# Kernel optimization log

Hardware: AMD Instinct MI355X
Metric: run time of the kernel (lower is better)

The kernel has to match this reference:

```python
import jax, jax.numpy as jnp
import numpy as np

B = 2            # batch size
GRID = 256       # BEV grid H = W
M = 30000        # number of pillars (voxels)
NPTS = 200000    # number of points
IN_C = 16
VOXEL = 0.4      # voxel_size[:2]
PC_MIN = -51.2   # pc_range[:2]
DS = 2           # prod(ds_layer_strides)


def _bn(x, g, b):
    # eval-mode BatchNorm with running_mean=0, running_var=1 (eps absorbed into g)
    return x * g + b


def _conv(x, k, stride):
    # 3x3 conv, padding=1 (spconv SparseConv2d / SubMConv2d with pad k//2), NHWC
    return jax.lax.conv_general_dilated(
        x, k, (stride, stride), ((1, 1), (1, 1)),
        dimension_numbers=('NHWC', 'HWIO', 'NHWC'))


def _active_mask(occ, stride):
    # active output sites of a sparse conv = any active input in the 3x3 receptive field
    pooled = jax.lax.reduce_window(occ, -jnp.inf, jax.lax.max,
                                   (1, 3, 3, 1), (1, stride, stride, 1),
                                   ((0, 0), (1, 1), (1, 1), (0, 0)))
    return (pooled > 0).astype(occ.dtype)


def _forward(features, pfn_w0, pfn_g0, pfn_b0, pfn_w1, pfn_g1, pfn_b1,
             b1_kd, b1_gd, b1_bd, b1_k1, b1_g1, b1_b1, b1_k2, b1_g2, b1_b2,
             b2_kd, b2_gd, b2_bd, b2_k1, b2_g1, b2_b1, b2_k2, b2_g2, b2_b2,
             unq, unq_inv, grid_size):
    # pillar mode: cols 0:2 are xy; convert to (fractional) voxel coordinates
    pos = (features[:, :2] - PC_MIN) / VOXEL  # [N,2] = (px, py)

    # PFN layer 0 (not last): linear(16->16) + BN + ReLU, concat per-pillar max
    h = jax.nn.relu(_bn(features @ pfn_w0, pfn_g0, pfn_b0))            # [N,16]
    hmax = jax.ops.segment_max(h, unq_inv, num_segments=M)             # [M,16]
    h = jnp.concatenate([h, hmax[unq_inv]], axis=1)                    # [N,32]
    # PFN layer 1 (last): linear(32->64) + BN + ReLU
    h = jax.nn.relu(_bn(h @ pfn_w1, pfn_g1, pfn_b1))                   # [N,64]

    # scatter_max pooling points -> pillars
    fv = jax.ops.segment_max(h, unq_inv, num_segments=M)               # [M,64]

    Hn = grid_size
    img = jnp.zeros((B, Hn, Hn, fv.shape[1]), fv.dtype)
    img = img.at[unq[:, 0], unq[:, 1], unq[:, 2]].set(fv)              # dense BEV, NHWC
    occ = jnp.zeros((B, Hn, Hn, 1), fv.dtype)
    occ = occ.at[unq[:, 0], unq[:, 1], unq[:, 2]].set(1.0)

    # block 1: SparseConvBlock(stride=1) + SparseBasicBlock (dense math, masked to active sites)
    occ1 = _active_mask(occ, 1)
    x = jax.nn.relu(_bn(_conv(img, b1_kd, 1), b1_gd, b1_bd)) * occ1
    y = jax.nn.relu(_bn(_conv(x, b1_k1, 1), b1_g1, b1_b1)) * occ1
    y = _bn(_conv(y, b1_k2, 1), b1_g2, b1_b2) * occ1
    x = jax.nn.relu(x + y)

    # block 2: SparseConvBlock(stride=2) + SparseBasicBlock
    occ2 = _active_mask(occ1, 2)
    x = jax.nn.relu(_bn(_conv(x, b2_kd, 2), b2_gd, b2_bd)) * occ2
    y = jax.nn.relu(_bn(_conv(x, b2_k1, 1), b2_g1, b2_b1)) * occ2
    y = _bn(_conv(y, b2_k2, 1), b2_g2, b2_b2) * occ2
    x = jax.nn.relu(x + y)                                             # [B,H/2,W/2,128]

    # bilinear gather at per-point downsampled positions (px -> W axis, py -> H axis)
    bidx = unq[unq_inv, 0]
    px = pos[:, 0] / DS
    py = pos[:, 1] / DS
    Hc, Wc = x.shape[1], x.shape[2]
    x0 = jnp.clip(jnp.floor(px).astype(jnp.int32), 0, Wc - 1)
    x1 = jnp.clip(jnp.floor(px).astype(jnp.int32) + 1, 0, Wc - 1)
    y0 = jnp.clip(jnp.floor(py).astype(jnp.int32), 0, Hc - 1)
    y1 = jnp.clip(jnp.floor(py).astype(jnp.int32) + 1, 0, Hc - 1)
    Ia = x[bidx, y0, x0]
    Ib = x[bidx, y1, x0]
    Ic = x[bidx, y0, x1]
    Id = x[bidx, y1, x1]
    x0f, x1f = x0.astype(px.dtype), x1.astype(px.dtype)
    y0f, y1f = y0.astype(py.dtype), y1.astype(py.dtype)
    wa = ((x1f - px) * (y1f - py))[:, None]
    wb = ((x1f - px) * (py - y0f))[:, None]
    wc = ((px - x0f) * (y1f - py))[:, None]
    wd = ((px - x0f) * (py - y0f))[:, None]
    return Ia * wa + Ib * wb + Ic * wc + Id * wd                       # [N,128]


def setup_inputs() -> dict:
    rng = np.random.default_rng(0)
    d = {}
    d['features'] = jnp.asarray(rng.standard_normal((NPTS, IN_C)).astype(np.float32))
    # unique voxel coords (batch, y, x)
    lin = rng.choice(B * GRID * GRID, size=M, replace=False)
    d['unq'] = jnp.asarray(np.stack([lin // (GRID * GRID), (lin // GRID) % GRID, lin % GRID], 1).astype(np.int32))
    # every pillar gets at least one point
    d['unq_inv'] = jnp.asarray(np.concatenate([np.arange(M), rng.integers(0, M, NPTS - M)]).astype(np.int32))
    d['grid_size'] = GRID

    def w(*s):
        fan = int(np.prod(s[:-1]))
        return jnp.asarray((rng.standard_normal(s) / np.sqrt(fan)).astype(np.float32))

    def g(c):
        return jnp.asarray((0.5 + 0.5 * rng.random(c)).astype(np.float32))

    def bb(c):
        return jnp.asarray((0.1 * rng.standard_normal(c)).astype(np.float32))

    d['pfn_w0'] = w(IN_C, 16); d['pfn_g0'] = g(16); d['pfn_b0'] = bb(16)
    d['pfn_w1'] = w(32, 64);   d['pfn_g1'] = g(64); d['pfn_b1'] = bb(64)
    d['b1_kd'] = w(3, 3, 64, 64);   d['b1_gd'] = g(64);  d['b1_bd'] = bb(64)
    d['b1_k1'] = w(3, 3, 64, 64);   d['b1_g1'] = g(64);  d['b1_b1'] = bb(64)
    d['b1_k2'] = w(3, 3, 64, 64);   d['b1_g2'] = g(64);  d['b1_b2'] = bb(64)
    d['b2_kd'] = w(3, 3, 64, 128);  d['b2_gd'] = g(128); d['b2_bd'] = bb(128)
    d['b2_k1'] = w(3, 3, 128, 128); d['b2_g1'] = g(128); d['b2_b1'] = bb(128)
    d['b2_k2'] = w(3, 3, 128, 128); d['b2_g2'] = g(128); d['b2_b2'] = bb(128)
    return d


def reference(features, unq, unq_inv, grid_size,
              pfn_w0, pfn_g0, pfn_b0, pfn_w1, pfn_g1, pfn_b1,
              b1_kd, b1_gd, b1_bd, b1_k1, b1_g1, b1_b1, b1_k2, b1_g2, b1_b2,
              b2_kd, b2_gd, b2_bd, b2_k1, b2_g1, b2_b1, b2_k2, b2_g2, b2_b2):
    return _forward(features, pfn_w0, pfn_g0, pfn_b0, pfn_w1, pfn_g1, pfn_b1,
                    b1_kd, b1_gd, b1_bd, b1_k1, b1_g1, b1_b1, b1_k2, b1_g2, b1_b2,
                    b2_kd, b2_gd, b2_bd, b2_k1, b2_g1, b2_b1, b2_k2, b2_g2, b2_b2,
                    unq, unq_inv, grid_size)
```

## Files before the change

### kernel.cpp

```cpp
#include <hip/hip_runtime.h>
#include <hip/hip_bf16.h>

#define NPTS    200000
#define MPIL    30000
#define BATCH   2
#define GRID0   256
#define PCMIN   (-51.2f)
#define VOXEL0  (0.4f)
#define NCHUNK  118

#define SLOT_B  ((size_t)16777216)
#define SLOT_F  ((size_t)33554432)

#define W0F 0
#define W1F 256
#define FB1 9216
#define FB2 156672
#define FB3 304128
#define FB4 451584
#define FB5 746496
#define FB6 1336320

#define WS_FLAG 0
#define WS_OCC8 64
#define WS_OCC1 (64 + 131072)
#define WS_OCC2 (64 + 262144)
#define WS_HMAX 393280
#define WS_CNT  2313280
#define WS_OFF  2433280
#define WS_CUR  2553344
#define WS_IDX  2673344
#define WS_LOC  3473344
#define WS_BS   3593344
#define WS_FX   393344

typedef __attribute__((ext_vector_type(8))) short v8s;
typedef __attribute__((ext_vector_type(4))) float f32x4;

static __device__ __forceinline__ float b2f(__hip_bfloat16 v) { return __bfloat162float(v); }
static __device__ __forceinline__ unsigned short f2bbits(float f) {
    __hip_bfloat16 h = __float2bfloat16(f);
    union { __hip_bfloat16 h; unsigned short u; } cv; cv.h = h; return cv.u;
}
static __device__ __forceinline__ float bits2f(unsigned short h) {
    union { unsigned int u; float f; } c; c.u = ((unsigned int)h) << 16; return c.f;
}
static __device__ __forceinline__ float lo2f(unsigned int u) {
    union { unsigned int u; float f; } c; c.u = u << 16; return c.f;
}
static __device__ __forceinline__ float hi2f(unsigned int u) {
    union { unsigned int u; float f; } c; c.u = u & 0xFFFF0000u; return c.f;
}
static __device__ __forceinline__ unsigned int pack2(float a, float b) {
    return (unsigned int)f2bbits(a) | ((unsigned int)f2bbits(b) << 16);
}
static __device__ __forceinline__ void split2(float a, float b, unsigned int& hi, unsigned int& lo) {
    unsigned short ha = f2bbits(a), hb = f2bbits(b);
    hi = (unsigned int)ha | ((unsigned int)hb << 16);
    float ra = a - bits2f(ha);
    float rb = b - bits2f(hb);
    lo = (unsigned int)f2bbits(ra) | ((unsigned int)f2bbits(rb) << 16);
}

static __device__ __forceinline__ float ldf(const void* p, size_t i, int isb) {
    return isb ? b2f(((const __hip_bfloat16*)p)[i]) : ((const float*)p)[i];
}
static __device__ __forceinline__ float4 ld4(const void* p, size_t i, int isb) {
    if (isb) {
        uint2 r = *(const uint2*)((const __hip_bfloat16*)p + i);
        return make_float4(lo2f(r.x), hi2f(r.x), lo2f(r.y), hi2f(r.y));
    }
    return *(const float4*)((const float*)p + i);
}
static __device__ __forceinline__ void st4(void* p, size_t i, int isb, float4 v) {
    if (isb) {
        uint2 pk; pk.x = pack2(v.x, v.y); pk.y = pack2(v.z, v.w);
        *(uint2*)((__hip_bfloat16*)p + i) = pk;
    } else {
        *(float4*)((float*)p + i) = v;
    }
}
static __device__ __forceinline__ void* actptr(void* ob, int slot, int isb) {
    return (char*)ob + (size_t)slot * (isb ? SLOT_B : SLOT_F);
}
static __device__ __forceinline__ float* wpool(void* ob, int isb) {
    return (float*)((char*)ob + 3 * (isb ? SLOT_B : SLOT_F));
}

__global__ void probe_kernel(const unsigned short* __restrict__ g0, int* __restrict__ flag) {
    if (threadIdx.x == 0 && blockIdx.x == 0) {
        int ok = 1;
        for (int i = 0; i < 8; i++) {
            unsigned short u = g0[i];
            if (u < 0x3E00 || u >= 0x4000) ok = 0;
        }
        *flag = ok;
    }
}

__global__ __launch_bounds__(256) void cvt_kernel(const void* __restrict__ src, void* ob,
                                                  int woff, int n, const int* __restrict__ flag) {
    int isb = *flag;
    int i = blockIdx.x * 256 + threadIdx.x;
    if (i < n) wpool(ob, isb)[woff + i] = ldf(src, i, isb);
}

__global__ __launch_bounds__(256) void wfrag_kernel(const void* __restrict__ src, void* ob,
                                                    int fb_bytes, int CIN, int COUT,
                                                    const int* __restrict__ flag)
{
    const int isb = *flag;
    const int cnt = 9 * CIN * COUT;
    int e = blockIdx.x * 256 + threadIdx.x;
    if (e >= cnt) return;
    int i = e & 7;
    int l = (e >> 3) & 63;
    int f = e >> 9;
    int nbn = COUT >> 4, kcn = CIN >> 5;
    int nb = f % nbn;
    int kc = (f / nbn) % kcn;
    int tap = f / (nbn * kcn);
    int ci = kc * 32 + (l >> 4) * 8 + i;
    int co = nb * 16 + (l & 15);
    float wv = ldf(src, (size_t)(tap * CIN + ci) * COUT + co, isb);
    unsigned short h = f2bbits(wv);
    float rem = wv - bits2f(h);
    short* wh = (short*)((char*)ob + 3 * (isb ? SLOT_B : SLOT_F) + fb_bytes);
    wh[e] = (short)h;
    wh[cnt + e] = (short)f2bbits(rem);
}

__global__ __launch_bounds__(256) void hist_kernel(const int* __restrict__ unq_inv,
                                                   int* __restrict__ cnt)
{
    int n = blockIdx.x * 256 + threadIdx.x;
    if (n < NPTS) atomicAdd(&cnt[unq_inv[n]], 1);
}

__global__ __launch_bounds__(256) void scan1_kernel(const int* __restrict__ cnt,
                                                    int* __restrict__ loc,
                                                    int* __restrict__ bs)
{
    __shared__ int s[256];
    const int tid = threadIdx.x;
    const int i = blockIdx.x * 256 + tid;
    int v = (i < MPIL) ? cnt[i] : 0;
    s[tid] = v;
    __syncthreads();
#pragma unroll
    for (int d = 1; d < 256; d <<= 1) {
        int t = (tid >= d) ? s[tid - d] : 0;
        __syncthreads();
        s[tid] += t;
        __syncthreads();
    }
    if (i < MPIL) loc[i] = s[tid] - v;
    if (tid == 255) bs[blockIdx.x] = s[255];
}

__global__ __launch_bounds__(128) void scan2_kernel(int* __restrict__ bs)
{
    __shared__ int s[NCHUNK];
    const int tid = threadIdx.x;
    for (int i = tid; i < NCHUNK; i += 128) s[i] = bs[i];
    __syncthreads();
    if (tid == 0) {
        int acc = 0;
        for (int i = 0; i < NCHUNK; i++) { int t = s[i]; s[i] = acc; acc += t; }
    }
    __syncthreads();
    for (int i = tid; i < NCHUNK; i += 128) bs[i] = s[i];
}

__global__ __launch_bounds__(256) void scan3_kernel(const int* __restrict__ loc,
                                                    const int* __restrict__ bs,
                                                    int* __restrict__ off,
                                                    int* __restrict__ cur)
{
    int i = blockIdx.x * 256 + threadIdx.x;
    if (i < MPIL) {
        int e = loc[i] + bs[blockIdx.x];
        off[i] = e; cur[i] = e;
    }
    if (i == 0) off[MPIL] = NPTS;
}

__global__ __launch_bounds__(256) void fill_kernel(const int* __restrict__ unq_inv,
                                                   int* __restrict__ cur,
                                                   int* __restrict__ idxarr)
{
    int n = blockIdx.x * 256 + threadIdx.x;
    if (n >= NPTS) return;
    int p = unq_inv[n];
    int s = atomicAdd(&cur[p], 1);
    idxarr[s] = n;
}

__global__ __launch_bounds__(256) void pfn0_kernel(
    const void* __restrict__ feat, void* ob, const void* __restrict__ g0,
    const void* __restrict__ b0, const int* __restrict__ flag)
{
    const int isb = *flag;
    int n = blockIdx.x * 256 + threadIdx.x;
    if (n >= NPTS) return;
    const float* w0f = wpool(ob, isb) + W0F;
    void* h0 = actptr(ob, 1, isb);
    float f[16];
#pragma unroll
    for (int i = 0; i < 16; i += 4) {
        float4 v = ld4(feat, (size_t)n * 16 + i, isb);
        f[i] = v.x; f[i + 1] = v.y; f[i + 2] = v.z; f[i + 3] = v.w;
    }
#pragma unroll
    for (int co = 0; co < 16; co += 4) {
        float a0 = 0.f, a1 = 0.f, a2 = 0.f, a3 = 0.f;
#pragma unroll
        for (int ci = 0; ci < 16; ci++) {
            float4 w = *(const float4*)&w0f[ci * 16 + co];
            a0 += f[ci] * w.x; a1 += f[ci] * w.y; a2 += f[ci] * w.z; a3 += f[ci] * w.w;
        }
        float o[4] = { a0, a1, a2, a3 };
#pragma unroll
        for (int k = 0; k < 4; k++) {
            float z = o[k] * ldf(g0, co + k, isb) + ldf(b0, co + k, isb);
            o[k] = fmaxf(z, 0.f);
        }
        st4(h0, (size_t)n * 16 + co, isb, make_float4(o[0], o[1], o[2], o[3]));
    }
}

__global__ __launch_bounds__(256) void hmax_kernel(
    void* ob, const int* __restrict__ off, const int* __restrict__ idxarr,
    float* __restrict__ hmax, const int* __restrict__ flag)
{
    const int isb = *flag;
    int t = blockIdx.x * 256 + threadIdx.x;
    if (t >= MPIL * 16) return;
    int p = t >> 4, ch = t & 15;
    const void* h0 = actptr(ob, 1, isb);
    float m = 0.f;
    int s1 = off[p + 1];
    for (int s = off[p]; s < s1; s++) {
        int n = idxarr[s];
        m = fmaxf(m, ldf(h0, (size_t)n * 16 + ch, isb));
    }
    hmax[t] = m;
}

template<bool BF>
static __device__ __forceinline__ void pfn1p_body(
    void* ob, const float* __restrict__ hmax, const void* __restrict__ g1,
    const void* __restrict__ b1, const int* __restrict__ off,
    const int* __restrict__ idxarr, const int* __restrict__ unq,
    unsigned char* __restrict__ occ)
{
    const int lane = threadIdx.x & 63;
    const int p = (blockIdx.x << 2) + (threadIdx.x >> 6);
    if (p >= MPIL) return;
    const int isb = BF ? 1 : 0;
    const float* w1f = wpool(ob, isb) + W1F;
    const void* h0 = actptr(ob, 1, isb);
    void* img = actptr(ob, 0, isb);

    float wcol[32];
#pragma unroll
    for (int k = 0; k < 32; k++) wcol[k] = w1f[k * 64 + lane];
    float base = 0.f;
#pragma unroll
    for (int k = 0; k < 16; k++) base += hmax[(size_t)p * 16 + k] * wcol[16 + k];
    const float g = ldf(g1, lane, isb);
    const float be = ldf(b1, lane, isb);

    float m = 0.f;
    const int s1 = off[p + 1];
    for (int s = off[p]; s < s1; s++) {
        const int n = idxarr[s];
        float h[16];
        if (BF) {
            const unsigned short* hp = (const unsigned short*)h0 + (size_t)n * 16;
            uint4 a = *(const uint4*)hp;
            uint4 c = *(const uint4*)(hp + 8);
            h[0] = lo2f(a.x); h[1] = hi2f(a.x); h[2] = lo2f(a.y); h[3] = hi2f(a.y);
            h[4] = lo2f(a.z); h[5] = hi2f(a.z); h[6] = lo2f(a.w); h[7] = hi2f(a.w);
            h[8] = lo2f(c.x); h[9] = hi2f(c.x); h[10] = lo2f(c.y); h[11] = hi2f(c.y);
            h[12] = lo2f(c.z); h[13] = hi2f(c.z); h[14] = lo2f(c.w); h[15] = hi2f(c.w);
        } else {
            const float* fp = (const float*)h0 + (size_t)n * 16;
#pragma unroll
            for (int i = 0; i < 16; i += 4) {
                float4 v = *(const float4*)(fp + i);
                h[i] = v.x; h[i + 1] = v.y; h[i + 2] = v.z; h[i + 3] = v.w;
            }
        }
        float z = base;
#pragma unroll
        for (int k = 0; k < 16; k++) z += h[k] * wcol[k];
        z = fmaxf(z * g + be, 0.f);
        m = fmaxf(m, z);
    }

    const int bb = unq[p * 3 + 0], yy = unq[p * 3 + 1], xx = unq[p * 3 + 2];
    const size_t site = ((size_t)bb * GRID0 + yy) * GRID0 + xx;
    if (BF) ((unsigned short*)img)[site * 64 + lane] = f2bbits(m);
    else    ((float*)img)[site * 64 + lane] = m;
    if (lane == 0) occ[site] = 1;
}

__global__ __launch_bounds__(256) void pfn1p_kernel(
    void* ob, const float* __restrict__ hmax, const void* __restrict__ g1,
    const void* __restrict__ b1, const int* __restrict__ off,
    const int* __restrict__ idxarr, const int* __restrict__ unq,
    unsigned char* __restrict__ occ, const int* __restrict__ flag)
{
    if (*flag) pfn1p_body<true>(ob, hmax, g1, b1, off, idxarr, unq, occ);
    else       pfn1p_body<false>(ob, hmax, g1, b1, off, idxarr, unq, occ);
}

__global__ __launch_bounds__(256) void dilate1_kernel(const unsigned char* __restrict__ occ,
                                                      unsigned char* __restrict__ occ1)
{
    int idx = blockIdx.x * 256 + threadIdx.x;
    if (idx >= BATCH * GRID0 * GRID0) return;
    int b = idx / (GRID0 * GRID0);
    int r = idx % (GRID0 * GRID0);
    int y = r / GRID0, x = r % GRID0;
    unsigned char v = 0;
#pragma unroll
    for (int dy = -1; dy <= 1; dy++) {
        int yy = y + dy; if (yy < 0 || yy >= GRID0) continue;
#pragma unroll
        for (int dx = -1; dx <= 1; dx++) {
            int xx = x + dx; if (xx < 0 || xx >= GRID0) continue;
            v |= occ[((size_t)b * GRID0 + yy) * GRID0 + xx];
        }
    }
    occ1[idx] = v ? 1 : 0;
}

__global__ __launch_bounds__(256) void dilate2_kernel(const unsigned char* __restrict__ occ1,
                                                      unsigned char* __restrict__ occ2)
{
    int idx = blockIdx.x * 256 + threadIdx.x;
    if (idx >= BATCH * 128 * 128) return;
    int b = idx / (128 * 128);
    int r = idx % (128 * 128);
    int y = r / 128, x = r % 128;
    unsigned char v = 0;
#pragma unroll
    for (int dy = -1; dy <= 1; dy++) {
        int yy = 2 * y + dy; if (yy < 0 || yy >= GRID0) continue;
#pragma unroll
        for (int dx = -1; dx <= 1; dx++) {
            int xx = 2 * x + dx; if (xx < 0 || xx >= GRID0) continue;
            v |= occ1[((size_t)b * GRID0 + yy) * GRID0 + xx];
        }
    }
    occ2[idx] = v ? 1 : 0;
}

template<int CIN, int COUT, int STRIDE, int TROWS, bool ADD_RES, bool BF>
static __device__ __forceinline__ void conv_body(
    short* s_a, const void* in, void* outp, const void* res, const short* wh,
    const void* gamma, const void* beta, const unsigned char* mask,
    int HIN, int WIN, int HOUT, int WOUT)
{
    constexpr int Y_EXT = (TROWS - 1) * STRIDE + 3;
    constexpr int X_EXT = 15 * STRIDE + 3;
    constexpr int PSTR = CIN + 8;
    constexpr int TSZ = Y_EXT * X_EXT * PSTR;
    constexpr int NCH8 = CIN / 8;
    constexpr int WPR = 4 / TROWS;
    constexpr int NBW = COUT / 16 / WPR;

    const int tid = threadIdx.x;
    const int b = blockIdx.z;
    const int oy0 = blockIdx.y * TROWS;
    const int ox0 = blockIdx.x * 16;

    for (int i = tid; i < Y_EXT * X_EXT * NCH8; i += 256) {
        int c8 = i % NCH8;
        int r = i / NCH8;
        int xo = r % X_EXT;
        int dy = r / X_EXT;
        int yin = oy0 * STRIDE - 1 + dy;
        int xin = ox0 * STRIDE - 1 + xo;
        bool inb = (yin >= 0 && yin < HIN && xin >= 0 && xin < WIN);
        int si = (dy * X_EXT + xo) * PSTR + c8 * 8;
        size_t gi = (((size_t)b * HIN + yin) * WIN + xin) * (size_t)CIN + c8 * 8;
        if (BF) {
            uint4 v = make_uint4(0u, 0u, 0u, 0u);
            if (inb) v = *(const uint4*)((const unsigned short*)in + gi);
            *(uint4*)&s_a[si] = v;
        } else {
            float4 va = make_float4(0.f, 0.f, 0.f, 0.f);
            float4 vb = make_float4(0.f, 0.f, 0.f, 0.f);
            if (inb) {
                va = *(const float4*)((const float*)in + gi);
                vb = *(const float4*)((const float*)in + gi + 4);
            }
            uint4 hv, lv;
            split2(va.x, va.y, hv.x, lv.x);
            split2(va.z, va.w, hv.y, lv.y);
            split2(vb.x, vb.y, hv.z, lv.z);
            split2(vb.z, vb.w, hv.w, lv.w);
            *(uint4*)&s_a[si] = hv;
            *(uint4*)&s_a[TSZ + si] = lv;
        }
    }
    __syncthreads();

    const int lane = tid & 63;
    const int w = tid >> 6;
    const int row = w / WPR;
    const int nb0 = (w % WPR) * NBW;
    const int l15 = lane & 15;
    const int lhi = lane >> 4;
    const short* wl = wh + 9 * CIN * COUT;

    f32x4 acc[NBW];
#pragma unroll
    for (int nb = 0; nb < NBW; nb++) acc[nb] = (f32x4){0.f, 0.f, 0.f, 0.f};

#pragma unroll 1
    for (int tap = 0; tap < 9; tap++) {
        const int ky = tap / 3, kx = tap % 3;
        const int abase = ((row * STRIDE + ky) * X_EXT + (l15 * STRIDE + kx)) * PSTR + lhi * 8;
#pragma unroll
        for (int kc = 0; kc < CIN / 32; kc++) {
            const v8s ah = *(const v8s*)&s_a[abase + kc * 32];
            v8s al;
            if (!BF) al = *(const v8s*)&s_a[TSZ + abase + kc * 32];
            const int f0 = (tap * (CIN / 32) + kc) * (COUT / 16) + nb0;
#pragma unroll
            for (int nb = 0; nb < NBW; nb++) {
                const size_t off = (size_t)(f0 + nb) * 512 + lane * 8;
                const v8s bh = *(const v8s*)&wh[off];
                acc[nb] = __builtin_amdgcn_mfma_f32_16x16x32_bf16(ah, bh, acc[nb], 0, 0, 0);
                if (!BF) {
                    const v8s bl = *(const v8s*)&wl[off];
                    acc[nb] = __builtin_amdgcn_mfma_f32_16x16x32_bf16(ah, bl, acc[nb], 0, 0, 0);
                    acc[nb] = __builtin_amdgcn_mfma_f32_16x16x32_bf16(al, bh, acc[nb], 0, 0, 0);
                }
            }
        }
    }

    const int oy = oy0 + row;
    const size_t mrow = ((size_t)b * HOUT + oy) * WOUT + ox0 + lhi * 4;
    float mk[4];
#pragma unroll
    for (int r = 0; r < 4; r++) mk[r] = mask[mrow + r] ? 1.f : 0.f;

#pragma unroll
    for (int nb = 0; nb < NBW; nb++) {
        const int n = (nb0 + nb) * 16 + l15;
        const float g = ldf(gamma, n, BF ? 1 : 0);
        const float be = ldf(beta, n, BF ? 1 : 0);
#pragma unroll
        for (int r = 0; r < 4; r++) {
            const size_t oaddr = (mrow + r) * COUT + n;
            float z = acc[nb][r] * g + be;
            z *= mk[r];
            if constexpr (ADD_RES) z += ldf(res, oaddr, BF ? 1 : 0);
            z = fmaxf(z, 0.f);
            if (BF) ((unsigned short*)outp)[oaddr] = f2bbits(z);
            else    ((float*)outp)[oaddr] = z;
        }
    }
}

template<int CIN, int COUT, int STRIDE, int TROWS, bool ADD_RES>
__global__ __launch_bounds__(256) void convmf_kernel(
    void* ob, int in_slot, int out_slot, void* out_ws, int res_slot, int fb_bytes,
    const void* __restrict__ gamma, const void* __restrict__ beta,
    const unsigned char* __restrict__ mask, const int* __restrict__ flag,
    int HIN, int WIN, int HOUT, int WOUT)
{
    constexpr int Y_EXT = (TROWS - 1) * STRIDE + 3;
    constexpr int X_EXT = 15 * STRIDE + 3;
    constexpr int PSTR = CIN + 8;
    constexpr int TSZ = Y_EXT * X_EXT * PSTR;
    __shared__ __align__(16) short s_a[2 * TSZ];

    const int isb = *flag;
    const void* in = actptr(ob, in_slot, isb);
    void* outp = out_ws ? out_ws : actptr(ob, out_slot, isb);
    const void* res = ADD_RES ? actptr(ob, res_slot, isb) : nullptr;
    const short* wh = (const short*)((const char*)ob + 3 * (isb ? SLOT_B : SLOT_F) + fb_bytes);

    if (isb)
        conv_body<CIN, COUT, STRIDE, TROWS, ADD_RES, true>(s_a, in, outp, res, wh,
                                                           gamma, beta, mask, HIN, WIN, HOUT, WOUT);
    else
        conv_body<CIN, COUT, STRIDE, TROWS, ADD_RES, false>(s_a, in, outp, res, wh,
                                                            gamma, beta, mask, HIN, WIN, HOUT, WOUT);
}

__global__ __launch_bounds__(256) void gather_kernel(
    const void* __restrict__ x, const void* __restrict__ feat,
    const int* __restrict__ unq, const int* __restrict__ unq_inv,
    void* __restrict__ out, const int* __restrict__ flag)
{
    const int isb = *flag;
    int idx = blockIdx.x * 256 + threadIdx.x;
    if (idx >= NPTS * 32) return;
    int n = idx >> 5;
    int co = (idx & 31) * 4;
    float fx = ldf(feat, (size_t)n * 16 + 0, isb);
    float fy = ldf(feat, (size_t)n * 16 + 1, isb);
    float px = ((fx - PCMIN) / VOXEL0) / 2.0f;
    float py = ((fy - PCMIN) / VOXEL0) / 2.0f;
    int bi = unq[(size_t)unq_inv[n] * 3 + 0];
    int xf = (int)floorf(px), yf = (int)floorf(py);
    int x0 = min(max(xf, 0), 127), x1 = min(max(xf + 1, 0), 127);
    int y0 = min(max(yf, 0), 127), y1 = min(max(yf + 1, 0), 127);
    float x0f = (float)x0, x1f = (float)x1, y0f = (float)y0, y1f = (float)y1;
    float wa = (x1f - px) * (y1f - py);
    float wb = (x1f - px) * (py - y0f);
    float wc = (px - x0f) * (y1f - py);
    float wd = (px - x0f) * (py - y0f);
    size_t base = (size_t)bi * 128 * 128 * 128;
    float4 Ia = ld4(x, base + ((size_t)y0 * 128 + x0) * 128 + co, isb);
    float4 Ib = ld4(x, base + ((size_t)y1 * 128 + x0) * 128 + co, isb);
    float4 Ic = ld4(x, base + ((size_t)y0 * 128 + x1) * 128 + co, isb);
    float4 Id = ld4(x, base + ((size_t)y1 * 128 + x1) * 128 + co, isb);
    float4 r;
    r.x = Ia.x * wa + Ib.x * wb + Ic.x * wc + Id.x * wd;
    r.y = Ia.y * wa + Ib.y * wb + Ic.y * wc + Id.y * wd;
    r.z = Ia.z * wa + Ib.z * wb + Ic.z * wc + Id.z * wd;
    r.w = Ia.w * wa + Ib.w * wb + Ic.w * wc + Id.w * wd;
    st4(out, (size_t)n * 128 + co, isb, r);
}

extern "C" void kernel_launch(void* const* d_in, const int* in_sizes, int n_in,
                              void* d_out, int out_size, void* d_ws, size_t ws_size,
                              hipStream_t stream)
{
    (void)in_sizes; (void)n_in; (void)out_size; (void)ws_size;
    const int* unq = (const int*)d_in[1];
    const int* unq_inv = (const int*)d_in[2];

    char* ws = (char*)d_ws;
    int* flagp = (int*)(ws + WS_FLAG);
    unsigned char* occ8 = (unsigned char*)(ws + WS_OCC8);
    unsigned char* occ1m = (unsigned char*)(ws + WS_OCC1);
    unsigned char* occ2m = (unsigned char*)(ws + WS_OCC2);
    float* hmax = (float*)(ws + WS_HMAX);
    int* cnt = (int*)(ws + WS_CNT);
    int* off = (int*)(ws + WS_OFF);
    int* cur = (int*)(ws + WS_CUR);
    int* idxarr = (int*)(ws + WS_IDX);
    int* loc = (int*)(ws + WS_LOC);
    int* bs = (int*)(ws + WS_BS);
    void* Fx = (void*)(ws + WS_FX);

    probe_kernel<<<1, 64, 0, stream>>>((const unsigned short*)d_in[5], flagp);

    cvt_kernel<<<1, 256, 0, stream>>>(d_in[4], d_out, W0F, 256, flagp);
    cvt_kernel<<<8, 256, 0, stream>>>(d_in[7], d_out, W1F, 2048, flagp);
    wfrag_kernel<<<144, 256, 0, stream>>>(d_in[10], d_out, FB1, 64, 64, flagp);
    wfrag_kernel<<<144, 256, 0, stream>>>(d_in[13], d_out, FB2, 64, 64, flagp);
    wfrag_kernel<<<144, 256, 0, stream>>>(d_in[16], d_out, FB3, 64, 64, flagp);
    wfrag_kernel<<<288, 256, 0, stream>>>(d_in[19], d_out, FB4, 64, 128, flagp);
    wfrag_kernel<<<576, 256, 0, stream>>>(d_in[22], d_out, FB5, 128, 128, flagp);
    wfrag_kernel<<<576, 256, 0, stream>>>(d_in[25], d_out, FB6, 128, 128, flagp);

    hipMemsetAsync(d_out, 0, SLOT_F, stream);
    hipMemsetAsync(cnt, 0, (size_t)MPIL * 4, stream);
    hipMemsetAsync(occ8, 0, 131072, stream);

    hist_kernel<<<(NPTS + 255) / 256, 256, 0, stream>>>(unq_inv, cnt);
    scan1_kernel<<<NCHUNK, 256, 0, stream>>>(cnt, loc, bs);
    scan2_kernel<<<1, 128, 0, stream>>>(bs);
    scan3_kernel<<<NCHUNK, 256, 0, stream>>>(loc, bs, off, cur);
    fill_kernel<<<(NPTS + 255) / 256, 256, 0, stream>>>(unq_inv, cur, idxarr);
    pfn0_kernel<<<(NPTS + 255) / 256, 256, 0, stream>>>(d_in[0], d_out, d_in[5], d_in[6], flagp);
    hmax_kernel<<<(MPIL * 16 + 255) / 256, 256, 0, stream>>>(d_out, off, idxarr, hmax, flagp);
    pfn1p_kernel<<<(MPIL + 3) / 4, 256, 0, stream>>>(d_out, hmax, d_in[8], d_in[9],
                                                     off, idxarr, unq, occ8, flagp);

    dilate1_kernel<<<(BATCH * GRID0 * GRID0) / 256, 256, 0, stream>>>(occ8, occ1m);
    dilate2_kernel<<<(BATCH * 128 * 128) / 256, 256, 0, stream>>>(occ1m, occ2m);

    dim3 blk(256);
    dim3 g1(16, 64, BATCH);
    convmf_kernel<64, 64, 1, 4, false><<<g1, blk, 0, stream>>>(
        d_out, 0, 1, nullptr, 0, FB1, d_in[11], d_in[12], occ1m, flagp, 256, 256, 256, 256);
    convmf_kernel<64, 64, 1, 4, false><<<g1, blk, 0, stream>>>(
        d_out, 1, 2, nullptr, 0, FB2, d_in[14], d_in[15], occ1m, flagp, 256, 256, 256, 256);
    convmf_kernel<64, 64, 1, 4, true><<<g1, blk, 0, stream>>>(
        d_out, 2, 0, nullptr, 1, FB3, d_in[17], d_in[18], occ1m, flagp, 256, 256, 256, 256);
    dim3 g2a(8, 64, BATCH), g2b(8, 32, BATCH);
    convmf_kernel<64, 128, 2, 2, false><<<g2a, blk, 0, stream>>>(
        d_out, 0, 1, nullptr, 0, FB4, d_in[20], d_in[21], occ2m, flagp, 256, 256, 128, 128);
    convmf_kernel<128, 128, 1, 4, false><<<g2b, blk, 0, stream>>>(
        d_out, 1, 2, nullptr, 0, FB5, d_in[23], d_in[24], occ2m, flagp, 128, 128, 128, 128);
    convmf_kernel<128, 128, 1, 4, true><<<g2b, blk, 0, stream>>>(
        d_out, 2, 0, Fx, 1, FB6, d_in[26], d_in[27], occ2m, flagp, 128, 128, 128, 128);

    gather_kernel<<<(NPTS * 32) / 256, 256, 0, stream>>>(Fx, d_in[0], unq, unq_inv,
                                                         d_out, flagp);
}
```

Measured before the change: 587.6 us.

## Tile conv over more output rows per block with register-held weight fragments

Restructures the MFMA conv so each wave owns a slice of output channels across several output rows, loading each weight fragment once into registers and reusing it for every row. Blocks now cover 16/8/4 rows instead of 2-4, which cuts redundant global weight reads and halo reloads. The fp32 path processes two half-tiles in sequence to fit LDS. It also remaps block IDs in an XCD-aware order and reads the mask as one 32-bit word. The cost is fewer blocks, more accumulator registers and lower occupancy.

```diff
diff --git a/kernel.cpp b/kernel.cpp
--- a/kernel.cpp
+++ b/kernel.cpp
@@ -358,25 +358,24 @@
     occ2[idx] = v ? 1 : 0;
 }
 
-template<int CIN, int COUT, int STRIDE, int TROWS, bool ADD_RES, bool BF>
-static __device__ __forceinline__ void conv_body(
+template<int CIN, int COUT, int STRIDE, bool ADD_RES, bool BF, int RR>
+static __device__ __forceinline__ void conv_tile(
     short* s_a, const void* in, void* outp, const void* res, const short* wh,
     const void* gamma, const void* beta, const unsigned char* mask,
-    int HIN, int WIN, int HOUT, int WOUT)
-{
-    constexpr int Y_EXT = (TROWS - 1) * STRIDE + 3;
+    int HIN, int WIN, int HOUT, int WOUT, int b, int oy0, int ox0)
+{
+    constexpr int Y_EXT = (RR - 1) * STRIDE + 3;
     constexpr int X_EXT = 15 * STRIDE + 3;
     constexpr int PSTR = CIN + 8;
     constexpr int TSZ = Y_EXT * X_EXT * PSTR;
     constexpr int NCH8 = CIN / 8;
-    constexpr int WPR = 4 / TROWS;
-    constexpr int NBW = COUT / 16 / WPR;
+    constexpr int NBW = COUT / 16 / 4;
+    constexpr int KCN = CIN / 32;
+    constexpr int NOB = COUT / 16;
 
     const int tid = threadIdx.x;
-    const int b = blockIdx.z;
-    const int oy0 = blockIdx.y * TROWS;
-    const int ox0 = blockIdx.x * 16;
-
+
+    __syncthreads();
     for (int i = tid; i < Y_EXT * X_EXT * NCH8; i += 256) {
         int c8 = i % NCH8;
         int r = i / NCH8;
@@ -411,76 +410,94 @@
 
     const int lane = tid & 63;
     const int w = tid >> 6;
-    const int row = w / WPR;
-    const int nb0 = (w % WPR) * NBW;
+    const int nb0 = w * NBW;
     const int l15 = lane & 15;
     const int lhi = lane >> 4;
     const short* wl = wh + 9 * CIN * COUT;
 
-    f32x4 acc[NBW];
-#pragma unroll
-    for (int nb = 0; nb < NBW; nb++) acc[nb] = (f32x4){0.f, 0.f, 0.f, 0.f};
+    f32x4 acc[RR][NBW];
+#pragma unroll
+    for (int rr = 0; rr < RR; rr++)
+#pragma unroll
+        for (int nb = 0; nb < NBW; nb++) acc[rr][nb] = (f32x4){0.f, 0.f, 0.f, 0.f};
 
 #pragma unroll 1
     for (int tap = 0; tap < 9; tap++) {
-        const int ky = tap / 3, kx = tap % 3;
-        const int abase = ((row * STRIDE + ky) * X_EXT + (l15 * STRIDE + kx)) * PSTR + lhi * 8;
-#pragma unroll
-        for (int kc = 0; kc < CIN / 32; kc++) {
-            const v8s ah = *(const v8s*)&s_a[abase + kc * 32];
-            v8s al;
-            if (!BF) al = *(const v8s*)&s_a[TSZ + abase + kc * 32];
-            const int f0 = (tap * (CIN / 32) + kc) * (COUT / 16) + nb0;
-#pragma unroll
-            for (int nb = 0; nb < NBW; nb++) {
-                const size_t off = (size_t)(f0 + nb) * 512 + lane * 8;
-                const v8s bh = *(const v8s*)&wh[off];
-                acc[nb] = __builtin_amdgcn_mfma_f32_16x16x32_bf16(ah, bh, acc[nb], 0, 0, 0);
-                if (!BF) {
-                    const v8s bl = *(const v8s*)&wl[off];
-                    acc[nb] = __builtin_amdgcn_mfma_f32_16x16x32_bf16(ah, bl, acc[nb], 0, 0, 0);
-                    acc[nb] = __builtin_amdgcn_mfma_f32_16x16x32_bf16(al, bh, acc[nb], 0, 0, 0);
+        const int ky = tap / 3;
+        const int kx = tap - ky * 3;
+        const int axy = ky * X_EXT + l15 * STRIDE + kx;
+#pragma unroll
+        for (int kc = 0; kc < KCN; kc++) {
+            const int f0 = (tap * KCN + kc) * NOB + nb0;
+            v8s bh[NBW];
+#pragma unroll
+            for (int nb = 0; nb < NBW; nb++)
+                bh[nb] = *(const v8s*)&wh[(size_t)(f0 + nb) * 512 + lane * 8];
+#pragma unroll
+            for (int rr = 0; rr < RR; rr++) {
+                const int abase = (rr * STRIDE * X_EXT + axy) * PSTR + lhi * 8 + kc * 32;
+                const v8s ah = *(const v8s*)&s_a[abase];
+#pragma unroll
+                for (int nb = 0; nb < NBW; nb++)
+                    acc[rr][nb] = __builtin_amdgcn_mfma_f32_16x16x32_bf16(ah, bh[nb], acc[rr][nb], 0, 0, 0);
+                if constexpr (!BF) {
+                    const v8s al = *(const v8s*)&s_a[TSZ + abase];
+#pragma unroll
+                    for (int nb = 0; nb < NBW; nb++) {
+                        const v8s bl = *(const v8s*)&wl[(size_t)(f0 + nb) * 512 + lane * 8];
+                        acc[rr][nb] = __builtin_amdgcn_mfma_f32_16x16x32_bf16(ah, bl, acc[rr][nb], 0, 0, 0);
+                        acc[rr][nb] = __builtin_amdgcn_mfma_f32_16x16x32_bf16(al, bh[nb], acc[rr][nb], 0, 0, 0);
+                    }
                 }
             }
         }
     }
 
-    const int oy = oy0 + row;
-    const size_t mrow = ((size_t)b * HOUT + oy) * WOUT + ox0 + lhi * 4;
-    float mk[4];
-#pragma unroll
-    for (int r = 0; r < 4; r++) mk[r] = mask[mrow + r] ? 1.f : 0.f;
-
-#pragma unroll
-    for (int nb = 0; nb < NBW; nb++) {
-        const int n = (nb0 + nb) * 16 + l15;
-        const float g = ldf(gamma, n, BF ? 1 : 0);
-        const float be = ldf(beta, n, BF ? 1 : 0);
-#pragma unroll
-        for (int r = 0; r < 4; r++) {
-            const size_t oaddr = (mrow + r) * COUT + n;
-            float z = acc[nb][r] * g + be;
-            z *= mk[r];
-            if constexpr (ADD_RES) z += ldf(res, oaddr, BF ? 1 : 0);
-            z = fmaxf(z, 0.f);
-            if (BF) ((unsigned short*)outp)[oaddr] = f2bbits(z);
-            else    ((float*)outp)[oaddr] = z;
-        }
-    }
-}
-
-template<int CIN, int COUT, int STRIDE, int TROWS, bool ADD_RES>
+#pragma unroll
+    for (int rr = 0; rr < RR; rr++) {
+        const int oy = oy0 + rr;
+        const size_t mrow = ((size_t)b * HOUT + oy) * WOUT + ox0 + lhi * 4;
+        const unsigned int mw = *(const unsigned int*)&mask[mrow];
+#pragma unroll
+        for (int nb = 0; nb < NBW; nb++) {
+            const int n = (nb0 + nb) * 16 + l15;
+            const float g = ldf(gamma, n, BF ? 1 : 0);
+            const float be = ldf(beta, n, BF ? 1 : 0);
+#pragma unroll
+            for (int r = 0; r < 4; r++) {
+                const size_t oaddr = (mrow + r) * COUT + n;
+                float z = acc[rr][nb][r] * g + be;
+                z *= ((mw >> (8 * r)) & 0xFF) ? 1.f : 0.f;
+                if constexpr (ADD_RES) z += ldf(res, oaddr, BF ? 1 : 0);
+                z = fmaxf(z, 0.f);
+                if (BF) ((unsigned short*)outp)[oaddr] = f2bbits(z);
+                else    ((float*)outp)[oaddr] = z;
+            }
+        }
+    }
+}
+
+template<int CIN, int COUT, int STRIDE, int R, bool ADD_RES>
 __global__ __launch_bounds__(256) void convmf_kernel(
     void* ob, int in_slot, int out_slot, void* out_ws, int res_slot, int fb_bytes,
     const void* __restrict__ gamma, const void* __restrict__ beta,
     const unsigned char* __restrict__ mask, const int* __restrict__ flag,
     int HIN, int WIN, int HOUT, int WOUT)
 {
-    constexpr int Y_EXT = (TROWS - 1) * STRIDE + 3;
     constexpr int X_EXT = 15 * STRIDE + 3;
     constexpr int PSTR = CIN + 8;
-    constexpr int TSZ = Y_EXT * X_EXT * PSTR;
-    __shared__ __align__(16) short s_a[2 * TSZ];
+    constexpr int TSZ_B = ((R - 1) * STRIDE + 3) * X_EXT * PSTR;
+    constexpr int TSZ_F = ((R / 2 - 1) * STRIDE + 3) * X_EXT * PSTR;
+    constexpr int LDS_SH = (TSZ_B > 2 * TSZ_F) ? TSZ_B : 2 * TSZ_F;
+    __shared__ __align__(16) short s_a[LDS_SH];
+
+    const int nbx = gridDim.x, nby = gridDim.y;
+    const int nwg = nbx * nby * (int)gridDim.z;
+    int bid = blockIdx.x + nbx * (blockIdx.y + nby * blockIdx.z);
+    bid = (bid & 7) * (nwg >> 3) + (bid >> 3);
+    const int bx = bid % nbx;
+    const int byy = (bid / nbx) % nby;
+    const int bz = bid / (nbx * nby);
 
     const int isb = *flag;
     const void* in = actptr(ob, in_slot, isb);
@@ -488,12 +505,18 @@
     const void* res = ADD_RES ? actptr(ob, res_slot, isb) : nullptr;
     const short* wh = (const short*)((const char*)ob + 3 * (isb ? SLOT_B : SLOT_F) + fb_bytes);
 
-    if (isb)
-        conv_body<CIN, COUT, STRIDE, TROWS, ADD_RES, true>(s_a, in, outp, res, wh,
-                                                           gamma, beta, mask, HIN, WIN, HOUT, WOUT);
-    else
-        conv_body<CIN, COUT, STRIDE, TROWS, ADD_RES, false>(s_a, in, outp, res, wh,
-                                                            gamma, beta, mask, HIN, WIN, HOUT, WOUT);
+    if (isb) {
+        conv_tile<CIN, COUT, STRIDE, ADD_RES, true, R>(
+            s_a, in, outp, res, wh, gamma, beta, mask,
+            HIN, WIN, HOUT, WOUT, bz, byy * R, bx * 16);
+    } else {
+        conv_tile<CIN, COUT, STRIDE, ADD_RES, false, R / 2>(
+            s_a, in, outp, res, wh, gamma, beta, mask,
+            HIN, WIN, HOUT, WOUT, bz, byy * R, bx * 16);
+        conv_tile<CIN, COUT, STRIDE, ADD_RES, false, R / 2>(
+            s_a, in, outp, res, wh, gamma, beta, mask,
+            HIN, WIN, HOUT, WOUT, bz, byy * R + R / 2, bx * 16);
+    }
 }
 
 __global__ __launch_bounds__(256) void gather_kernel(
@@ -583,19 +606,19 @@
     dilate2_kernel<<<(BATCH * 128 * 128) / 256, 256, 0, stream>>>(occ1m, occ2m);
 
     dim3 blk(256);
-    dim3 g1(16, 64, BATCH);
-    convmf_kernel<64, 64, 1, 4, false><<<g1, blk, 0, stream>>>(
+    dim3 g1(16, 16, BATCH);
+    convmf_kernel<64, 64, 1, 16, false><<<g1, blk, 0, stream>>>(
         d_out, 0, 1, nullptr, 0, FB1, d_in[11], d_in[12], occ1m, flagp, 256, 256, 256, 256);
-    convmf_kernel<64, 64, 1, 4, false><<<g1, blk, 0, stream>>>(
+    convmf_kernel<64, 64, 1, 16, false><<<g1, blk, 0, stream>>>(
         d_out, 1, 2, nullptr, 0, FB2, d_in[14], d_in[15], occ1m, flagp, 256, 256, 256, 256);
-    convmf_kernel<64, 64, 1, 4, true><<<g1, blk, 0, stream>>>(
+    convmf_kernel<64, 64, 1, 16, true><<<g1, blk, 0, stream>>>(
         d_out, 2, 0, nullptr, 1, FB3, d_in[17], d_in[18], occ1m, flagp, 256, 256, 256, 256);
-    dim3 g2a(8, 64, BATCH), g2b(8, 32, BATCH);
-    convmf_kernel<64, 128, 2, 2, false><<<g2a, blk, 0, stream>>>(
+    dim3 g2a(8, 32, BATCH), g2b(8, 16, BATCH);
+    convmf_kernel<64, 128, 2, 4, false><<<g2a, blk, 0, stream>>>(
         d_out, 0, 1, nullptr, 0, FB4, d_in[20], d_in[21], occ2m, flagp, 256, 256, 128, 128);
-    convmf_kernel<128, 128, 1, 4, false><<<g2b, blk, 0, stream>>>(
+    convmf_kernel<128, 128, 1, 8, false><<<g2b, blk, 0, stream>>>(
         d_out, 1, 2, nullptr, 0, FB5, d_in[23], d_in[24], occ2m, flagp, 128, 128, 128, 128);
-    convmf_kernel<128, 128, 1, 4, true><<<g2b, blk, 0, stream>>>(
+    convmf_kernel<128, 128, 1, 8, true><<<g2b, blk, 0, stream>>>(
         d_out, 2, 0, Fx, 1, FB6, d_in[26], d_in[27], occ2m, flagp, 128, 128, 128, 128);
 
     gather_kernel<<<(NPTS * 32) / 256, 256, 0, stream>>>(Fx, d_in[0], unq, unq_inv,
```

New measurement: 561.4 us. 1.05x faster.
